# Performance work log

Measured on AMD Instinct MI355X. Metric: run time of the kernel, lower is better.

## Reference

```python
import jax, jax.numpy as jnp
from jax import lax
import numpy as np

T = 8
TAU = 2.0       # LIFNode tau
VTH = 1.0       # v_threshold for IF and LIF
ALPHA = 2.0     # surrogate.ATan default alpha
BN_EPS = 1e-5

# --- ATan surrogate-gradient heaviside (spikingjelly semantics) ---
@jax.custom_vjp
def heaviside_atan(x):
    return (x >= 0.0).astype(x.dtype)

def _h_fwd(x):
    return heaviside_atan(x), x

def _h_bwd(x, g):
    sg = (ALPHA / 2.0) / (1.0 + (jnp.pi / 2.0 * ALPHA * x) ** 2)
    return (g * sg,)

heaviside_atan.defvjp(_h_fwd, _h_bwd)

# --- multi-step IF node: v += x; spike; hard reset to 0 ---
def if_node(x_seq):
    def step(v, x):
        v = v + x
        s = heaviside_atan(v - VTH)
        return (1.0 - s) * v, s
    return lax.scan(step, jnp.zeros_like(x_seq[0]), x_seq)[1]

# --- multi-step LIF node (decay_input=True, v_reset=0, hard reset) ---
def lif_node(x_seq):
    def step(v, x):
        v = v + (x - v) / TAU
        s = heaviside_atan(v - VTH)
        return (1.0 - s) * v, s
    return lax.scan(step, jnp.zeros_like(x_seq[0]), x_seq)[1]

def conv2d(x, w, b):
    y = lax.conv_general_dilated(x, w, (1, 1), 'SAME', dimension_numbers=('NCHW', 'OIHW', 'NCHW'))
    return y + b[None, :, None, None]

def bn(x, g, b, m, v):
    scale = g * lax.rsqrt(v + BN_EPS)
    return (x - m[None, :, None, None]) * scale[None, :, None, None] + b[None, :, None, None]

def maxpool2(x):
    return lax.reduce_window(x, -jnp.inf, lax.max, (1, 1, 2, 2), (1, 1, 2, 2), 'VALID')


def setup_inputs():
    key = jax.random.key(0)
    ks = jax.random.split(key, 8)
    B = 32
    f32 = jnp.float32
    d = {}
    d['x'] = jax.random.normal(ks[0], (B, 1, 48, 48), f32)
    d['conv1_w'] = jax.random.normal(ks[1], (128, 1, 3, 3), f32) * 0.2
    d['conv1_b'] = jnp.zeros((128,), f32)
    d['bn1_g'] = jnp.ones((128,), f32)
    d['bn1_b'] = jnp.zeros((128,), f32)
    d['bn1_m'] = jnp.zeros((128,), f32)
    d['bn1_v'] = jnp.ones((128,), f32)
    d['conv2_w'] = jax.random.normal(ks[2], (128, 128, 3, 3), f32) * 0.03
    d['conv2_b'] = jnp.zeros((128,), f32)
    d['bn2_g'] = jnp.ones((128,), f32)
    d['bn2_b'] = jnp.zeros((128,), f32)
    d['bn2_m'] = jnp.zeros((128,), f32)
    d['bn2_v'] = jnp.ones((128,), f32)
    d['fc1_w'] = jax.random.normal(ks[3], (1152, 128 * 12 * 12), f32) * 0.007
    d['fc1_b'] = jnp.zeros((1152,), f32)
    d['fc2_w'] = jax.random.normal(ks[4], (128, 1152), f32) * 0.03
    d['fc2_b'] = jnp.zeros((128,), f32)
    d['fc3_w'] = jax.random.normal(ks[5], (7, 128), f32) * 0.09
    d['fc3_b'] = jnp.zeros((7,), f32)
    return d


def reference(x, conv1_w, conv1_b, bn1_g, bn1_b, bn1_m, bn1_v,
              conv2_w, conv2_b, bn2_g, bn2_b, bn2_m, bn2_v,
              fc1_w, fc1_b, fc2_w, fc2_b, fc3_w, fc3_b):
    B = x.shape[0]
    # layer1 (single-step): conv + BN (eval-mode), dropout is identity at eval
    h = bn(conv2d(x, conv1_w, conv1_b), bn1_g, bn1_b, bn1_m, bn1_v)  # [B,128,48,48]
    # repeat over T timesteps
    x_step = jnp.broadcast_to(h, (T,) + h.shape)                      # [T,B,128,48,48]
    # layer2: IF -> maxpool -> conv -> BN -> IF -> maxpool
    s1 = if_node(x_step)                                              # [T,B,128,48,48]
    p1 = maxpool2(s1.reshape((T * B,) + s1.shape[2:]))                # [T*B,128,24,24]
    c2 = bn(conv2d(p1, conv2_w, conv2_b), bn2_g, bn2_b, bn2_m, bn2_v)
    s2 = if_node(c2.reshape((T, B) + c2.shape[1:]))                   # [T,B,128,24,24]
    p2 = maxpool2(s2.reshape((T * B,) + s2.shape[2:]))                # [T*B,128,12,12]
    # layer3: flatten -> fc -> LIF -> fc -> LIF -> fc -> LIF
    f = p2.reshape(T, B, -1)                                          # [T,B,18432]
    l1 = lif_node(jnp.einsum('tbi,oi->tbo', f, fc1_w) + fc1_b)        # [T,B,1152]
    l2 = lif_node(jnp.einsum('tbi,oi->tbo', l1, fc2_w) + fc2_b)       # [T,B,128]
    l3 = lif_node(jnp.einsum('tbi,oi->tbo', l2, fc3_w) + fc3_b)       # [T,B,7]
    return l3.mean(axis=0)                                            # [B,7]
```

## Files before the change

kernel.cpp:

```cpp
#include <hip/hip_runtime.h>
#include <hip/hip_bf16.h>


typedef float  f32x4  __attribute__((ext_vector_type(4)));
typedef __bf16 bf16x8 __attribute__((ext_vector_type(8)));

#define T_STEPS 8

static const size_t OFF_P1    = 0;
static const size_t OFF_PART  = 0;
static const size_t OFF_WT    = 44302336;
static const size_t OFF_P2    = 45481984;
static const size_t OFF_W2T   = 54919168;
static const size_t OFF_L1S   = 55508992;

__device__ __forceinline__ unsigned short bf16_rne(float f) {
  unsigned u = __builtin_bit_cast(unsigned, f);
  u += 0x7FFFu + ((u >> 16) & 1u);
  return (unsigned short)(u >> 16);
}
__device__ __forceinline__ float bf16_to_f(unsigned short h) {
  unsigned u = ((unsigned)h) << 16;
  return __builtin_bit_cast(float, u);
}

__device__ __forceinline__ void split_pair(float f0, float f1, unsigned& hi, unsigned& lo) {
  __hip_bfloat162 h2 = __float22bfloat162_rn(make_float2(f0, f1));
  unsigned uh; __builtin_memcpy(&uh, &h2, 4);
  float g0 = __builtin_bit_cast(float, uh << 16);
  float g1 = __builtin_bit_cast(float, uh & 0xFFFF0000u);
  __hip_bfloat162 l2 = __float22bfloat162_rn(make_float2(f0 - g0, f1 - g1));
  unsigned ul; __builtin_memcpy(&ul, &l2, 4);
  hi = uh;
  lo = ul;
}

__device__ __forceinline__ void lds_load16(const void* g, void* l) {
  auto* gp = reinterpret_cast<const __attribute__((address_space(1))) unsigned int*>(
      reinterpret_cast<uintptr_t>(g));
  auto* lp = reinterpret_cast<__attribute__((address_space(3))) unsigned int*>(
      reinterpret_cast<uintptr_t>(l));
  __builtin_amdgcn_global_load_lds(gp, lp, 16, 0, 0);
}

__global__ __launch_bounds__(256) void prep(const float* __restrict__ conv2_w,
                                            const float* __restrict__ fc2_w,
                                            short* __restrict__ wt_hi,
                                            short* __restrict__ wt_lo,
                                            float* __restrict__ w2t,
                                            uint4* __restrict__ p1pad4) {
  int i = blockIdx.x * 256 + threadIdx.x;
  if (i < 147456) {
    int tap = i >> 14;
    int oc  = (i >> 7) & 127;
    int ic  = i & 127;
    float wv = conv2_w[oc * 1152 + ic * 9 + tap];
    unsigned short h = bf16_rne(wv);
    wt_hi[i] = (short)h;
    wt_lo[i] = (short)bf16_rne(wv - bf16_to_f(h));
  } else if (i < 294912) {
    int j = i - 147456;
    int o = j & 127, k = j >> 7;
    w2t[j] = fc2_w[o * 1152 + k];
  } else if (i < 704512) {
    int k = i - 294912;
    int tb = k / 1600;
    int rem = k - tb * 1600;
    int pos = rem >> 4, c8 = rem & 15;
    int y, x;
    if (pos < 26)      { y = 0;  x = pos; }
    else if (pos < 52) { y = 25; x = pos - 26; }
    else { int jj = pos - 52; y = 1 + (jj >> 1); x = (jj & 1) * 25; }
    p1pad4[(tb * 676 + y * 26 + x) * 16 + c8] = make_uint4(0u, 0u, 0u, 0u);
  }
}

__global__ __launch_bounds__(128) void conv1_if_pool(
    const float* __restrict__ x, const float* __restrict__ w1, const float* __restrict__ b1,
    const float* __restrict__ g1, const float* __restrict__ be1, const float* __restrict__ m1,
    const float* __restrict__ vv1, short* __restrict__ p1) {
  __shared__ float patch[16];
  const int c  = threadIdx.x;
  const int sp = blockIdx.x;
  const int b  = blockIdx.y;
  const int oy = sp / 24, ox = sp % 24;
  if (c < 16) {
    int py = c >> 2, px = c & 3;
    int iy = 2 * oy - 1 + py, ix = 2 * ox - 1 + px;
    float v = 0.f;
    if (iy >= 0 && iy < 48 && ix >= 0 && ix < 48) v = x[b * 2304 + iy * 48 + ix];
    patch[c] = v;
  }
  __syncthreads();
  float w[9];
#pragma unroll
  for (int i = 0; i < 9; ++i) w[i] = w1[c * 9 + i];
  float scale = g1[c] * rsqrtf(vv1[c] + 1e-5f);
  float shift = (b1[c] - m1[c]) * scale + be1[c];
  float h[4];
#pragma unroll
  for (int p = 0; p < 4; ++p) {
    int py = p >> 1, px = p & 1;
    float s = 0.f;
#pragma unroll
    for (int dy = 0; dy < 3; ++dy)
#pragma unroll
      for (int dx = 0; dx < 3; ++dx) s += patch[(py + dy) * 4 + (px + dx)] * w[dy * 3 + dx];
    h[p] = s * scale + shift;
  }
  float va = 0.f, vb = 0.f, vc = 0.f, vd = 0.f;
  size_t base = ((size_t)b * 676 + (size_t)(1 + oy) * 26 + (1 + ox)) * 128 + c;
#pragma unroll
  for (int t = 0; t < T_STEPS; ++t) {
    va += h[0]; vb += h[1]; vc += h[2]; vd += h[3];
    bool s0 = va >= 1.f, s1 = vb >= 1.f, s2 = vc >= 1.f, s3 = vd >= 1.f;
    p1[base + (size_t)t * (32 * 676 * 128)] = (s0 | s1 | s2 | s3) ? (short)0x3F80 : (short)0;
    if (s0) va = 0.f; if (s1) vb = 0.f; if (s2) vc = 0.f; if (s3) vd = 0.f;
  }
}

__global__ __launch_bounds__(256, 4) void conv2_gemm(
    const short* __restrict__ p1pad, const short* __restrict__ wt_hi, const short* __restrict__ wt_lo,
    const float* __restrict__ conv2_b, const float* __restrict__ bn2_g, const float* __restrict__ bn2_b,
    const float* __restrict__ bn2_m, const float* __restrict__ bn2_v, short* __restrict__ p2) {
  __shared__ __align__(16) short lds[12288];
  short* ldsA  = lds;
  short* ldsBh = lds + 4096;
  short* ldsBl = lds + 8192;

  const int tid = threadIdx.x;
  const int lane = tid & 63;
  const int w = tid >> 6;
  const int wm = w & 1, wn = w >> 1;
  const int b = blockIdx.y;
  const int gy = blockIdx.x / 3;
  const int gx = blockIdx.x - gy * 3;

  int rowofsA[2], bofs[2];
#pragma unroll
  for (int j = 0; j < 2; ++j) {
    int r = j * 64 + w * 16 + (lane >> 2);
    int t = r >> 4, iy = (r >> 3) & 1, ix = r & 7;
    rowofsA[j] = (((t * 32 + b) * 676) + (2 * gy + iy) * 26 + (8 * gx + ix)) * 128 + (lane & 3) * 8;
    bofs[j] = r * 128 + (lane & 3) * 8;
  }

  f32x4 acc[4][4];
#pragma unroll
  for (int mi = 0; mi < 4; ++mi)
#pragma unroll
    for (int ni = 0; ni < 4; ++ni) acc[mi][ni] = (f32x4){0.f, 0.f, 0.f, 0.f};

#pragma unroll 1
  for (int s = 0; s < 36; ++s) {
    const int tap = s >> 2;
    const int kk = (s & 3) << 5;
    const int tapoff = ((tap / 3) * 26 + (tap % 3)) * 128;
    __syncthreads();
#pragma unroll
    for (int j = 0; j < 2; ++j) {
      lds_load16(p1pad + rowofsA[j] + tapoff + kk, ldsA + (j * 64 + w * 16) * 32 + lane * 8);
    }
    const int wtoff = tap * 16384 + kk;
#pragma unroll
    for (int j = 0; j < 2; ++j) {
      lds_load16(wt_hi + wtoff + bofs[j], ldsBh + (j * 64 + w * 16) * 32 + lane * 8);
      lds_load16(wt_lo + wtoff + bofs[j], ldsBl + (j * 64 + w * 16) * 32 + lane * 8);
    }
    __syncthreads();
    const int cch = lane >> 4;
    bf16x8 a[4], bh[4], bl[4];
#pragma unroll
    for (int i = 0; i < 4; ++i) {
      int r = wm * 64 + i * 16 + (lane & 15);
      a[i] = *(const bf16x8*)(ldsA + r * 32 + cch * 8);
      int n = wn * 64 + i * 16 + (lane & 15);
      bh[i] = *(const bf16x8*)(ldsBh + n * 32 + cch * 8);
      bl[i] = *(const bf16x8*)(ldsBl + n * 32 + cch * 8);
    }
#pragma unroll
    for (int mi = 0; mi < 4; ++mi)
#pragma unroll
      for (int ni = 0; ni < 4; ++ni) {
        acc[mi][ni] = __builtin_amdgcn_mfma_f32_16x16x32_bf16(a[mi], bh[ni], acc[mi][ni], 0, 0, 0);
        acc[mi][ni] = __builtin_amdgcn_mfma_f32_16x16x32_bf16(a[mi], bl[ni], acc[mi][ni], 0, 0, 0);
      }
  }

  float sc[4], sh[4];
#pragma unroll
  for (int ni = 0; ni < 4; ++ni) {
    int oc = wn * 64 + ni * 16 + (lane & 15);
    sc[ni] = bn2_g[oc] * rsqrtf(bn2_v[oc] + 1e-5f);
    sh[ni] = (conv2_b[oc] - bn2_m[oc]) * sc[ni] + bn2_b[oc];
  }
  float* ybuf = (float*)lds;
  const int S = 132;
  float v[16];
#pragma unroll
  for (int q = 0; q < 16; ++q) v[q] = 0.f;
  unsigned short* p2u = (unsigned short*)p2;
  __syncthreads();
#pragma unroll
  for (int q = 0; q < 4; ++q) {
    if (wm == (q >> 1)) {
#pragma unroll
      for (int ml = 0; ml < 2; ++ml) {
        const int mi = (q & 1) * 2 + ml;
#pragma unroll
        for (int ni = 0; ni < 4; ++ni)
#pragma unroll
          for (int r = 0; r < 4; ++r) {
            int lam = ml * 16 + ((lane >> 4) << 2) + r;
            int col = wn * 64 + ni * 16 + (lane & 15);
            ybuf[lam * S + col] = acc[mi][ni][r] * sc[ni] + sh[ni];
          }
      }
    }
    __syncthreads();
    if (tid < 128) {
      const int oc = tid;
#pragma unroll
      for (int tt = 0; tt < 2; ++tt) {
        int t = 2 * q + tt;
        unsigned short ov[4];
#pragma unroll
        for (int px = 0; px < 4; ++px) {
          bool any = false;
#pragma unroll
          for (int iy = 0; iy < 2; ++iy)
#pragma unroll
            for (int rx = 0; rx < 2; ++rx) {
              int pos = iy * 8 + 2 * px + rx;
              float xx = ybuf[(tt * 16 + pos) * S + oc];
              v[pos] += xx;
              bool ss = v[pos] >= 1.f;
              any |= ss;
              if (ss) v[pos] = 0.f;
            }
          ov[px] = any ? (unsigned short)0x3F80 : (unsigned short)0;
        }
        ushort4 o4; o4.x = ov[0]; o4.y = ov[1]; o4.z = ov[2]; o4.w = ov[3];
        *(ushort4*)(p2u + ((size_t)(t * 32 + b) * 128 + oc) * 144 + gy * 12 + gx * 4) = o4;
      }
    }
    __syncthreads();
  }
}

__global__ __launch_bounds__(512) void fc1_gemm(const short* __restrict__ p2,
                                                const float* __restrict__ fc1_w,
                                                float* __restrict__ part) {
  __shared__ __align__(16) short lds[32768];
  short* ldsA = lds;
  short* ldsBh = lds + 16384;
  short* ldsBl = lds + 24576;

  const int tid = threadIdx.x;
  const int lane = tid & 63;
  const int w = tid >> 6;
  const int wm = w & 3, wn = w >> 2;
  const int n0 = blockIdx.x * 128;
  const int kb = blockIdx.y * 576;

  const int g = (lane & 7) ^ (lane >> 3);
  int aofs[4];
#pragma unroll
  for (int j = 0; j < 4; ++j) {
    int r = w * 32 + j * 8 + (lane >> 3);
    aofs[j] = r * 18432 + g * 8;
  }
  const int bn = tid >> 2;
  const int c0 = (tid & 3) * 2;
  const float* wrow = fc1_w + (size_t)(n0 + bn) * 18432 + c0 * 8;
  const int bpos0 = (c0 ^ (bn & 7)) * 8;
  const int bpos1 = ((c0 + 1) ^ (bn & 7)) * 8;

  f32x4 acc[4][4];
#pragma unroll
  for (int mi = 0; mi < 4; ++mi)
#pragma unroll
    for (int ni = 0; ni < 4; ++ni) acc[mi][ni] = (f32x4){0.f, 0.f, 0.f, 0.f};

#pragma unroll 1
  for (int s = 0; s < 9; ++s) {
    const int koff = kb + s * 64;
    __syncthreads();
#pragma unroll
    for (int j = 0; j < 4; ++j) {
      lds_load16(p2 + aofs[j] + koff, ldsA + (w * 32 + j * 8) * 64 + lane * 8);
    }
    {
      const float4* wp = (const float4*)(wrow + koff);
      float4 q0 = wp[0], q1 = wp[1], q2 = wp[2], q3 = wp[3];
      unsigned h0, h1, h2, h3, h4, h5, h6, h7;
      unsigned l0, l1, l2, l3, l4, l5, l6, l7;
      split_pair(q0.x, q0.y, h0, l0);
      split_pair(q0.z, q0.w, h1, l1);
      split_pair(q1.x, q1.y, h2, l2);
      split_pair(q1.z, q1.w, h3, l3);
      split_pair(q2.x, q2.y, h4, l4);
      split_pair(q2.z, q2.w, h5, l5);
      split_pair(q3.x, q3.y, h6, l6);
      split_pair(q3.z, q3.w, h7, l7);
      uint4 H0; H0.x = h0; H0.y = h1; H0.z = h2; H0.w = h3;
      uint4 H1; H1.x = h4; H1.y = h5; H1.z = h6; H1.w = h7;
      uint4 L0; L0.x = l0; L0.y = l1; L0.z = l2; L0.w = l3;
      uint4 L1; L1.x = l4; L1.y = l5; L1.z = l6; L1.w = l7;
      *(uint4*)(ldsBh + bn * 64 + bpos0) = H0;
      *(uint4*)(ldsBh + bn * 64 + bpos1) = H1;
      *(uint4*)(ldsBl + bn * 64 + bpos0) = L0;
      *(uint4*)(ldsBl + bn * 64 + bpos1) = L1;
    }
    __syncthreads();
#pragma unroll
    for (int ks = 0; ks < 2; ++ks) {
      bf16x8 a[4], bh[4], bl[4];
      const int cch = ks * 4 + (lane >> 4);
#pragma unroll
      for (int i = 0; i < 4; ++i) {
        int r = wm * 64 + i * 16 + (lane & 15);
        a[i] = *(const bf16x8*)(ldsA + r * 64 + ((cch ^ (r & 7)) * 8));
        int n = wn * 64 + i * 16 + (lane & 15);
        bh[i] = *(const bf16x8*)(ldsBh + n * 64 + ((cch ^ (n & 7)) * 8));
        bl[i] = *(const bf16x8*)(ldsBl + n * 64 + ((cch ^ (n & 7)) * 8));
      }
#pragma unroll
      for (int mi = 0; mi < 4; ++mi)
#pragma unroll
        for (int ni = 0; ni < 4; ++ni) {
          acc[mi][ni] = __builtin_amdgcn_mfma_f32_16x16x32_bf16(a[mi], bh[ni], acc[mi][ni], 0, 0, 0);
          acc[mi][ni] = __builtin_amdgcn_mfma_f32_16x16x32_bf16(a[mi], bl[ni], acc[mi][ni], 0, 0, 0);
        }
    }
  }
  const size_t pbase = (size_t)(blockIdx.y * 9 + blockIdx.x) * 32768;
#pragma unroll
  for (int ni = 0; ni < 4; ++ni) {
    int j = wn * 64 + ni * 16 + (lane & 15);
#pragma unroll
    for (int mi = 0; mi < 4; ++mi) {
#pragma unroll
      for (int r = 0; r < 4; ++r) {
        int m = wm * 64 + mi * 16 + ((lane >> 4) << 2) + r;
        part[pbase + (size_t)m * 128 + j] = acc[mi][ni][r];
      }
    }
  }
}

__global__ __launch_bounds__(128) void fc1_reduce_lif(const float* __restrict__ part,
                                                      const float* __restrict__ fc1_b,
                                                      float* __restrict__ l1s) {
  int i = blockIdx.x * 128 + threadIdx.x;
  int b = i / 1152, n = i - b * 1152;
  int nt = n >> 7, j = n & 127;
  float bias = fc1_b[n];
  float v = 0.f;
#pragma unroll
  for (int t = 0; t < T_STEPS; ++t) {
    int m = t * 32 + b;
    float s = bias;
#pragma unroll 8
    for (int ks = 0; ks < 32; ++ks) s += part[(((size_t)ks * 9 + nt) * 256 + m) * 128 + j];
    v += (s - v) * 0.5f;
    bool sp = v >= 1.f;
    l1s[(size_t)m * 1152 + n] = sp ? 1.f : 0.f;
    if (sp) v = 0.f;
  }
}

__global__ __launch_bounds__(512) void tail(const float* __restrict__ l1s,
                                            const float* __restrict__ w2t,
                                            const float* __restrict__ b2,
                                            const float* __restrict__ w3,
                                            const float* __restrict__ b3,
                                            float* __restrict__ out) {
  __shared__ float sx[8][1152];
  __shared__ float part2[4][8][128];
  __shared__ float s2[8][128];
  __shared__ float y3[7][8];
  const int b = blockIdx.x;
  const int tid = threadIdx.x;
  for (int i = tid; i < 9216; i += 512) {
    int t = i / 1152, k = i - t * 1152;
    sx[t][k] = l1s[(size_t)(t * 32 + b) * 1152 + k];
  }
  __syncthreads();
  const int o = tid & 127, h = tid >> 7;
  float p[8];
#pragma unroll
  for (int t = 0; t < 8; ++t) p[t] = 0.f;
#pragma unroll 4
  for (int kk = 0; kk < 288; ++kk) {
    int k = h * 288 + kk;
    float wv = w2t[k * 128 + o];
#pragma unroll
    for (int t = 0; t < 8; ++t) p[t] += sx[t][k] * wv;
  }
#pragma unroll
  for (int t = 0; t < 8; ++t) part2[h][t][o] = p[t];
  __syncthreads();
  if (tid < 128) {
    float v = 0.f;
#pragma unroll
    for (int t = 0; t < 8; ++t) {
      float xx = part2[0][t][o] + part2[1][t][o] + part2[2][t][o] + part2[3][t][o] + b2[o];
      v += (xx - v) * 0.5f;
      bool s = v >= 1.f;
      s2[t][o] = s ? 1.f : 0.f;
      if (s) v = 0.f;
    }
  }
  __syncthreads();
  if (tid < 56) {
    int oo = tid >> 3, t = tid & 7;
    float d = 0.f;
    for (int k = 0; k < 128; ++k) d += s2[t][k] * w3[oo * 128 + k];
    y3[oo][t] = d + b3[oo];
  }
  __syncthreads();
  if (tid < 7) {
    float v = 0.f, a = 0.f;
#pragma unroll
    for (int t = 0; t < 8; ++t) {
      float xx = y3[tid][t];
      v += (xx - v) * 0.5f;
      bool s = v >= 1.f;
      a += s ? 1.f : 0.f;
      if (s) v = 0.f;
    }
    out[b * 7 + tid] = a * 0.125f;
  }
}

extern "C" void kernel_launch(void* const* d_in, const int* in_sizes, int n_in,
                              void* d_out, int out_size, void* d_ws, size_t ws_size,
                              hipStream_t stream) {
  const float* x       = (const float*)d_in[0];
  const float* conv1_w = (const float*)d_in[1];
  const float* conv1_b = (const float*)d_in[2];
  const float* bn1_g   = (const float*)d_in[3];
  const float* bn1_b   = (const float*)d_in[4];
  const float* bn1_m   = (const float*)d_in[5];
  const float* bn1_v   = (const float*)d_in[6];
  const float* conv2_w = (const float*)d_in[7];
  const float* conv2_b = (const float*)d_in[8];
  const float* bn2_g   = (const float*)d_in[9];
  const float* bn2_b   = (const float*)d_in[10];
  const float* bn2_m   = (const float*)d_in[11];
  const float* bn2_v   = (const float*)d_in[12];
  const float* fc1_w   = (const float*)d_in[13];
  const float* fc1_b   = (const float*)d_in[14];
  const float* fc2_w   = (const float*)d_in[15];
  const float* fc2_b   = (const float*)d_in[16];
  const float* fc3_w   = (const float*)d_in[17];
  const float* fc3_b   = (const float*)d_in[18];

  char* ws = (char*)d_ws;
  short* p1pad = (short*)(ws + OFF_P1);
  float* part  = (float*)(ws + OFF_PART);
  short* wt_hi = (short*)(ws + OFF_WT);
  short* wt_lo = wt_hi + 147456;
  short* p2    = (short*)(ws + OFF_P2);
  float* w2t   = (float*)(ws + OFF_W2T);
  float* l1s   = (float*)(ws + OFF_L1S);
  float* out   = (float*)d_out;

  prep<<<2752, 256, 0, stream>>>(conv2_w, fc2_w, wt_hi, wt_lo, w2t, (uint4*)p1pad);
  conv1_if_pool<<<dim3(576, 32), 128, 0, stream>>>(x, conv1_w, conv1_b, bn1_g, bn1_b, bn1_m, bn1_v, p1pad);
  conv2_gemm<<<dim3(36, 32), 256, 0, stream>>>(p1pad, wt_hi, wt_lo, conv2_b, bn2_g, bn2_b, bn2_m, bn2_v, p2);
  fc1_gemm<<<dim3(9, 32), 512, 0, stream>>>(p2, fc1_w, part);
  fc1_reduce_lif<<<288, 128, 0, stream>>>(part, fc1_b, l1s);
  tail<<<32, 512, 0, stream>>>(l1s, w2t, fc2_b, fc3_w, fc3_b, out);
}
```

Baseline: 378.6 us.

## Fuse prep with conv1, swizzle conv2 LDS layout, split conv2 launch

Merges the weight-prep/padding kernel and the conv1+IF+pool kernel into one launch, with conv1 blocks processing two spatial positions per 256-thread block. Adds an XOR swizzle to the conv2 GEMM's LDS tile layout so fragment reads hit fewer bank conflicts. Splits the conv2 launch into two half-batch launches and raises the unroll factor in the fc1 reduction. The fused kernel has no ordering between the pad-zeroing and conv1 writes, but they touch disjoint regions; the extra launch adds overhead.

```diff
diff --git a/kernel.cpp b/kernel.cpp
--- a/kernel.cpp
+++ b/kernel.cpp
@@ -43,53 +43,56 @@
   __builtin_amdgcn_global_load_lds(gp, lp, 16, 0, 0);
 }
 
-__global__ __launch_bounds__(256) void prep(const float* __restrict__ conv2_w,
-                                            const float* __restrict__ fc2_w,
-                                            short* __restrict__ wt_hi,
-                                            short* __restrict__ wt_lo,
-                                            float* __restrict__ w2t,
-                                            uint4* __restrict__ p1pad4) {
-  int i = blockIdx.x * 256 + threadIdx.x;
-  if (i < 147456) {
-    int tap = i >> 14;
-    int oc  = (i >> 7) & 127;
-    int ic  = i & 127;
-    float wv = conv2_w[oc * 1152 + ic * 9 + tap];
-    unsigned short h = bf16_rne(wv);
-    wt_hi[i] = (short)h;
-    wt_lo[i] = (short)bf16_rne(wv - bf16_to_f(h));
-  } else if (i < 294912) {
-    int j = i - 147456;
-    int o = j & 127, k = j >> 7;
-    w2t[j] = fc2_w[o * 1152 + k];
-  } else if (i < 704512) {
-    int k = i - 294912;
-    int tb = k / 1600;
-    int rem = k - tb * 1600;
-    int pos = rem >> 4, c8 = rem & 15;
-    int y, x;
-    if (pos < 26)      { y = 0;  x = pos; }
-    else if (pos < 52) { y = 25; x = pos - 26; }
-    else { int jj = pos - 52; y = 1 + (jj >> 1); x = (jj & 1) * 25; }
-    p1pad4[(tb * 676 + y * 26 + x) * 16 + c8] = make_uint4(0u, 0u, 0u, 0u);
-  }
-}
-
-__global__ __launch_bounds__(128) void conv1_if_pool(
-    const float* __restrict__ x, const float* __restrict__ w1, const float* __restrict__ b1,
-    const float* __restrict__ g1, const float* __restrict__ be1, const float* __restrict__ m1,
+__global__ __launch_bounds__(256) void prep_conv1(
+    const float* __restrict__ conv2_w, const float* __restrict__ fc2_w,
+    short* __restrict__ wt_hi, short* __restrict__ wt_lo,
+    float* __restrict__ w2t, uint4* __restrict__ p1pad4,
+    const float* __restrict__ x, const float* __restrict__ w1,
+    const float* __restrict__ b1, const float* __restrict__ g1,
+    const float* __restrict__ be1, const float* __restrict__ m1,
     const float* __restrict__ vv1, short* __restrict__ p1) {
-  __shared__ float patch[16];
-  const int c  = threadIdx.x;
-  const int sp = blockIdx.x;
-  const int b  = blockIdx.y;
+  __shared__ float patch[2][16];
+  const int blk = blockIdx.x;
+  if (blk < 2752) {
+    int i = blk * 256 + threadIdx.x;
+    if (i < 147456) {
+      int tap = i >> 14;
+      int oc  = (i >> 7) & 127;
+      int ic  = i & 127;
+      float wv = conv2_w[oc * 1152 + ic * 9 + tap];
+      unsigned short h = bf16_rne(wv);
+      wt_hi[i] = (short)h;
+      wt_lo[i] = (short)bf16_rne(wv - bf16_to_f(h));
+    } else if (i < 294912) {
+      int j = i - 147456;
+      int o = j & 127, k = j >> 7;
+      w2t[j] = fc2_w[o * 1152 + k];
+    } else if (i < 704512) {
+      int k = i - 294912;
+      int tb = k / 1600;
+      int rem = k - tb * 1600;
+      int pos = rem >> 4, c8 = rem & 15;
+      int y, xx;
+      if (pos < 26)      { y = 0;  xx = pos; }
+      else if (pos < 52) { y = 25; xx = pos - 26; }
+      else { int jj = pos - 52; y = 1 + (jj >> 1); xx = (jj & 1) * 25; }
+      p1pad4[(tb * 676 + y * 26 + xx) * 16 + c8] = make_uint4(0u, 0u, 0u, 0u);
+    }
+    return;
+  }
+  const int idx = blk - 2752;
+  const int b = idx / 288;
+  const int sp2 = idx - b * 288;
+  const int half = threadIdx.x >> 7;
+  const int c = threadIdx.x & 127;
+  const int sp = sp2 * 2 + half;
   const int oy = sp / 24, ox = sp % 24;
   if (c < 16) {
     int py = c >> 2, px = c & 3;
     int iy = 2 * oy - 1 + py, ix = 2 * ox - 1 + px;
     float v = 0.f;
     if (iy >= 0 && iy < 48 && ix >= 0 && ix < 48) v = x[b * 2304 + iy * 48 + ix];
-    patch[c] = v;
+    patch[half][c] = v;
   }
   __syncthreads();
   float w[9];
@@ -105,7 +108,7 @@
 #pragma unroll
     for (int dy = 0; dy < 3; ++dy)
 #pragma unroll
-      for (int dx = 0; dx < 3; ++dx) s += patch[(py + dy) * 4 + (px + dx)] * w[dy * 3 + dx];
+      for (int dx = 0; dx < 3; ++dx) s += patch[half][(py + dy) * 4 + (px + dx)] * w[dy * 3 + dx];
     h[p] = s * scale + shift;
   }
   float va = 0.f, vb = 0.f, vc = 0.f, vd = 0.f;
@@ -122,7 +125,8 @@
 __global__ __launch_bounds__(256, 4) void conv2_gemm(
     const short* __restrict__ p1pad, const short* __restrict__ wt_hi, const short* __restrict__ wt_lo,
     const float* __restrict__ conv2_b, const float* __restrict__ bn2_g, const float* __restrict__ bn2_b,
-    const float* __restrict__ bn2_m, const float* __restrict__ bn2_v, short* __restrict__ p2) {
+    const float* __restrict__ bn2_m, const float* __restrict__ bn2_v, short* __restrict__ p2,
+    int boff) {
   __shared__ __align__(16) short lds[12288];
   short* ldsA  = lds;
   short* ldsBh = lds + 4096;
@@ -132,17 +136,18 @@
   const int lane = tid & 63;
   const int w = tid >> 6;
   const int wm = w & 1, wn = w >> 1;
-  const int b = blockIdx.y;
+  const int b = boff + blockIdx.y;
   const int gy = blockIdx.x / 3;
   const int gx = blockIdx.x - gy * 3;
 
+  const int cs = (lane & 3) ^ ((lane >> 3) & 3);
   int rowofsA[2], bofs[2];
 #pragma unroll
   for (int j = 0; j < 2; ++j) {
     int r = j * 64 + w * 16 + (lane >> 2);
     int t = r >> 4, iy = (r >> 3) & 1, ix = r & 7;
-    rowofsA[j] = (((t * 32 + b) * 676) + (2 * gy + iy) * 26 + (8 * gx + ix)) * 128 + (lane & 3) * 8;
-    bofs[j] = r * 128 + (lane & 3) * 8;
+    rowofsA[j] = (((t * 32 + b) * 676) + (2 * gy + iy) * 26 + (8 * gx + ix)) * 128 + cs * 8;
+    bofs[j] = r * 128 + cs * 8;
   }
 
   f32x4 acc[4][4];
@@ -173,10 +178,10 @@
 #pragma unroll
     for (int i = 0; i < 4; ++i) {
       int r = wm * 64 + i * 16 + (lane & 15);
-      a[i] = *(const bf16x8*)(ldsA + r * 32 + cch * 8);
+      a[i] = *(const bf16x8*)(ldsA + r * 32 + ((cch ^ ((r >> 1) & 3)) * 8));
       int n = wn * 64 + i * 16 + (lane & 15);
-      bh[i] = *(const bf16x8*)(ldsBh + n * 32 + cch * 8);
-      bl[i] = *(const bf16x8*)(ldsBl + n * 32 + cch * 8);
+      bh[i] = *(const bf16x8*)(ldsBh + n * 32 + ((cch ^ ((n >> 1) & 3)) * 8));
+      bl[i] = *(const bf16x8*)(ldsBl + n * 32 + ((cch ^ ((n >> 1) & 3)) * 8));
     }
 #pragma unroll
     for (int mi = 0; mi < 4; ++mi)
@@ -361,7 +366,7 @@
   for (int t = 0; t < T_STEPS; ++t) {
     int m = t * 32 + b;
     float s = bias;
-#pragma unroll 8
+#pragma unroll 16
     for (int ks = 0; ks < 32; ++ks) s += part[(((size_t)ks * 9 + nt) * 256 + m) * 128 + j];
     v += (s - v) * 0.5f;
     bool sp = v >= 1.f;
@@ -467,9 +472,10 @@
   float* l1s   = (float*)(ws + OFF_L1S);
   float* out   = (float*)d_out;
 
-  prep<<<2752, 256, 0, stream>>>(conv2_w, fc2_w, wt_hi, wt_lo, w2t, (uint4*)p1pad);
-  conv1_if_pool<<<dim3(576, 32), 128, 0, stream>>>(x, conv1_w, conv1_b, bn1_g, bn1_b, bn1_m, bn1_v, p1pad);
-  conv2_gemm<<<dim3(36, 32), 256, 0, stream>>>(p1pad, wt_hi, wt_lo, conv2_b, bn2_g, bn2_b, bn2_m, bn2_v, p2);
+  prep_conv1<<<11968, 256, 0, stream>>>(conv2_w, fc2_w, wt_hi, wt_lo, w2t, (uint4*)p1pad,
+                                        x, conv1_w, conv1_b, bn1_g, bn1_b, bn1_m, bn1_v, p1pad);
+  conv2_gemm<<<dim3(36, 16), 256, 0, stream>>>(p1pad, wt_hi, wt_lo, conv2_b, bn2_g, bn2_b, bn2_m, bn2_v, p2, 0);
+  conv2_gemm<<<dim3(36, 16), 256, 0, stream>>>(p1pad, wt_hi, wt_lo, conv2_b, bn2_g, bn2_b, bn2_m, bn2_v, p2, 16);
   fc1_gemm<<<dim3(9, 32), 512, 0, stream>>>(p2, fc1_w, part);
   fc1_reduce_lif<<<288, 128, 0, stream>>>(part, fc1_b, l1s);
   tail<<<32, 512, 0, stream>>>(l1s, w2t, fc2_b, fc3_w, fc3_b, out);
```

After: 376.0 us. About the same (-0.7%).
